# Performance work log

Measured on AMD Instinct MI355X. Metric: run time of the kernel, lower is better.

The kernel has to match this reference:

```python
import jax, jax.numpy as jnp
import numpy as np

D_MODEL = 1024
HEAD_DIM = 256
MEMORY_SIZE = 64
SPARSITY_RATIO = 0.1
NEG_INF = -1.0e9


def setup_inputs() -> dict:
    key = jax.random.key(0)
    ks = jax.random.split(key, 16)
    s = lambda fan_in: 1.0 / np.sqrt(fan_in)
    inp = {
        "x": jax.random.normal(ks[0], (2, 4096, D_MODEL), dtype=jnp.float32),
        # local attention head (qkv fused, no bias); weights stored [in, out]
        "local_qkv_w": jax.random.uniform(ks[1], (D_MODEL, 3 * HEAD_DIM), minval=-s(D_MODEL), maxval=s(D_MODEL)),
        # sparse global head
        "sparse_qkv_w": jax.random.uniform(ks[2], (D_MODEL, 3 * HEAD_DIM), minval=-s(D_MODEL), maxval=s(D_MODEL)),
        # memory head
        "memory_bank": jax.random.normal(ks[3], (MEMORY_SIZE, HEAD_DIM), dtype=jnp.float32),
        "memory_proj_w": jax.random.uniform(ks[4], (D_MODEL, HEAD_DIM), minval=-s(D_MODEL), maxval=s(D_MODEL)),
        "mem_out_w": jax.random.uniform(ks[5], (2 * HEAD_DIM, HEAD_DIM), minval=-s(2 * HEAD_DIM), maxval=s(2 * HEAD_DIM)),
        "mem_out_b": jax.random.uniform(ks[6], (HEAD_DIM,), minval=-s(2 * HEAD_DIM), maxval=s(2 * HEAD_DIM)),
        # prediction head
        "pred_in_w": jax.random.uniform(ks[7], (D_MODEL, HEAD_DIM), minval=-s(D_MODEL), maxval=s(D_MODEL)),
        "pred_in_b": jax.random.uniform(ks[8], (HEAD_DIM,), minval=-s(D_MODEL), maxval=s(D_MODEL)),
        "pred1_w": jax.random.uniform(ks[9], (HEAD_DIM, 2 * HEAD_DIM), minval=-s(HEAD_DIM), maxval=s(HEAD_DIM)),
        "pred1_b": jax.random.uniform(ks[10], (2 * HEAD_DIM,), minval=-s(HEAD_DIM), maxval=s(HEAD_DIM)),
        "pred2_w": jax.random.uniform(ks[11], (2 * HEAD_DIM, HEAD_DIM), minval=-s(2 * HEAD_DIM), maxval=s(2 * HEAD_DIM)),
        "pred2_b": jax.random.uniform(ks[12], (HEAD_DIM,), minval=-s(2 * HEAD_DIM), maxval=s(2 * HEAD_DIM)),
        # warboss output projection
        "warboss_w": jax.random.uniform(ks[13], (4 * HEAD_DIM, D_MODEL), minval=-s(4 * HEAD_DIM), maxval=s(4 * HEAD_DIM)),
        "warboss_b": jax.random.uniform(ks[14], (D_MODEL,), minval=-s(4 * HEAD_DIM), maxval=s(4 * HEAD_DIM)),
    }
    return inp


def _full_attention(x, qkv_w, scale):
    # x: [B,S,D] -> q,k,v: [B,S,H]
    qkv = x @ qkv_w
    q, k, v = jnp.split(qkv, 3, axis=-1)
    scores = jnp.einsum("bsh,bth->bst", q, k) * scale  # [B,S,S]
    probs = jax.nn.softmax(scores, axis=-1)
    return probs @ v


def _sparse_global_attention(x, qkv_w, scale):
    qkv = x @ qkv_w
    q, k, v = jnp.split(qkv, 3, axis=-1)
    scores = jnp.einsum("bsh,bth->bst", q, k) * scale  # [B,S,S]
    seq_len = x.shape[1]
    k_sparse = max(1, int(seq_len * SPARSITY_RATIO))
    topk_vals, _ = jax.lax.top_k(scores, k_sparse)
    kth = topk_vals[..., -1:]  # [B,S,1] threshold
    masked = jnp.where(scores >= kth, scores, NEG_INF)
    probs = jax.nn.softmax(masked, axis=-1)
    return probs @ v


def _memory_head(x, memory_bank, memory_proj_w, mem_out_w, mem_out_b):
    x_proj = x @ memory_proj_w  # [B,S,H]
    mem_scores = jnp.einsum("bsh,mh->bsm", x_proj, memory_bank)
    mem_weights = jax.nn.softmax(mem_scores, axis=-1)
    retrieved = jnp.einsum("bsm,mh->bsh", mem_weights, memory_bank)
    combined = jnp.concatenate([x_proj, retrieved], axis=-1)
    return combined @ mem_out_w + mem_out_b


def _prediction_head(x, pred_in_w, pred_in_b, pred1_w, pred1_b, pred2_w, pred2_b):
    h = x @ pred_in_w + pred_in_b
    h = h @ pred1_w + pred1_b
    h = jax.nn.gelu(h, approximate=False)
    return h @ pred2_w + pred2_b


def reference(x, local_qkv_w, sparse_qkv_w, memory_bank, memory_proj_w, mem_out_w, mem_out_b, pred_in_w, pred_in_b, pred1_w, pred1_b, pred2_w, pred2_b, warboss_w, warboss_b):
    scale = HEAD_DIM ** -0.5
    local_out = _full_attention(x, local_qkv_w, scale)
    sparse_out = _sparse_global_attention(x, sparse_qkv_w, scale)
    mem_out = _memory_head(x, memory_bank, memory_proj_w, mem_out_w, mem_out_b)
    pred_out = _prediction_head(x, pred_in_w, pred_in_b, pred1_w, pred1_b, pred2_w, pred2_b)
    combined = jnp.concatenate([local_out, sparse_out, mem_out, pred_out], axis=-1)
    return combined @ warboss_w + warboss_b
```

## Files before the change

kernel.cpp:

```cpp
#include <hip/hip_runtime.h>
#include <hip/hip_bf16.h>

typedef __attribute__((ext_vector_type(8))) _Float16 half8;
typedef __attribute__((ext_vector_type(4))) _Float16 half4v;
typedef __attribute__((ext_vector_type(4))) float f32x4;

__device__ __forceinline__ float wred_max(float v){
  #pragma unroll
  for (int o = 32; o; o >>= 1) v = fmaxf(v, __shfl_xor(v, o));
  return v;
}
__device__ __forceinline__ float wred_sum(float v){
  #pragma unroll
  for (int o = 32; o; o >>= 1) v += __shfl_xor(v, o);
  return v;
}
__device__ __forceinline__ unsigned short h2u(_Float16 h){
  unsigned short u;
  __builtin_memcpy(&u, &h, 2);
  return u;
}
__device__ __forceinline__ float u2hf(unsigned short u){
  _Float16 h;
  __builtin_memcpy(&h, &u, 2);
  return (float)h;
}

#define GLOAD16(GP, LP) __builtin_amdgcn_global_load_lds( \
    (const __attribute__((address_space(1))) void*)(GP),  \
    (__attribute__((address_space(3))) void*)(LP), 16, 0, 0)

template<int BM, int BN, int OUT_F16, int ACT>
__global__ __launch_bounds__(256) void gemm_ht(
    const _Float16* __restrict__ A, long saz, int lda,
    const _Float16* __restrict__ B, long sbz, int ldb,
    void* __restrict__ Cv, long scz, int ldc,
    int K, float alpha, const float* __restrict__ bias)
{
  constexpr int FM = BM / 32, FN = BN / 32;
  __shared__ __align__(16) _Float16 Asl[BM * 32];
  __shared__ __align__(16) _Float16 Bsl[BN * 32];
  const int t = threadIdx.x;
  const int wid = t >> 6, lane = t & 63;
  const int wr = wid >> 1, wc = wid & 1;
  const int lr = lane & 15, kg = lane >> 4;
  A += (long)blockIdx.z * saz;
  B += (long)blockIdx.z * sbz;
  const long row0 = (long)blockIdx.y * BM;
  const long col0 = (long)blockIdx.x * BN;

  f32x4 acc[FM][FN];
  #pragma unroll
  for (int i = 0; i < FM; i++)
    #pragma unroll
    for (int j = 0; j < FN; j++)
      acc[i][j] = (f32x4){0.f, 0.f, 0.f, 0.f};

  const int arow_t = t >> 2, acol_t = (t & 3) * 8;

  for (int k0 = 0; k0 < K; k0 += 32){
    #pragma unroll
    for (int r = 0; r < BM / 64; r++){
      const _Float16* gp = A + (row0 + r*64 + arow_t) * (long)lda + k0 + acol_t;
      GLOAD16(gp, (char*)Asl + r*4096 + wid*1024);
    }
    #pragma unroll
    for (int r = 0; r < BN / 64; r++){
      const _Float16* gp = B + (col0 + r*64 + arow_t) * (long)ldb + k0 + acol_t;
      GLOAD16(gp, (char*)Bsl + r*4096 + wid*1024);
    }
    __syncthreads();
    half8 af[FM], bfv[FN];
    #pragma unroll
    for (int i = 0; i < FM; i++)
      af[i] = *(const half8*)((const char*)Asl + (wr*(BM/2) + i*16 + lr)*64 + kg*16);
    #pragma unroll
    for (int j = 0; j < FN; j++)
      bfv[j] = *(const half8*)((const char*)Bsl + (wc*(BN/2) + j*16 + lr)*64 + kg*16);
    #pragma unroll
    for (int i = 0; i < FM; i++)
      #pragma unroll
      for (int j = 0; j < FN; j++)
        acc[i][j] = __builtin_amdgcn_mfma_f32_16x16x32_f16(af[i], bfv[j], acc[i][j], 0, 0, 0);
    __syncthreads();
  }

  _Float16* Ch = (_Float16*)Cv + (long)blockIdx.z * scz;
  float*    Cf = (float*)Cv    + (long)blockIdx.z * scz;
  #pragma unroll
  for (int i = 0; i < FM; i++){
    #pragma unroll
    for (int j = 0; j < FN; j++){
      #pragma unroll
      for (int q = 0; q < 4; q++){
        long rr = row0 + wr*(BM/2) + i*16 + kg*4 + q;
        long cc = col0 + wc*(BN/2) + j*16 + lr;
        float val = acc[i][j][q] * alpha;
        if (bias) val += bias[cc];
        if constexpr (ACT) val = 0.5f * val * (1.0f + erff(val * 0.70710678118654752f));
        if constexpr (OUT_F16) Ch[rr*(long)ldc + cc] = (_Float16)val;
        else                   Cf[rr*(long)ldc + cc] = val;
      }
    }
  }
}

template<int BM, int BN, int SPARSE>
__global__ __launch_bounds__(256) void gemm_pv_exp(
    const _Float16* __restrict__ A, long saz, int lda,
    const _Float16* __restrict__ B, long sbz, int ldb,
    const float4* __restrict__ mlthr,
    _Float16* __restrict__ Ph, int nsplit, int Ksplit)
{
  constexpr int FM = BM / 32, FN = BN / 32;
  __shared__ __align__(16) _Float16 Asl[BM * 32];
  __shared__ __align__(16) _Float16 Bsl[BN * 32];
  const int t = threadIdx.x;
  const int wid = t >> 6, lane = t & 63;
  const int wr = wid >> 1, wc = wid & 1;
  const int lr = lane & 15, kg = lane >> 4;
  const int z = blockIdx.z, batch = z / nsplit, split = z % nsplit;
  A += (long)batch * saz;
  B += (long)batch * sbz;
  _Float16* Pz = Ph + (size_t)z * (4096 * 256);
  const long row0 = (long)blockIdx.y * BM;
  const int Kbase = split * Ksplit;

  const long arow = row0 + (t >> 2);
  const float4 mt = mlthr[(long)batch*4096 + arow];
  const float m = mt.x, thr = mt.z;
  const _Float16* Ap = A + arow * (long)lda + Kbase + (t & 3) * 8;

  f32x4 acc[FM][FN];
  #pragma unroll
  for (int i = 0; i < FM; i++)
    #pragma unroll
    for (int j = 0; j < FN; j++)
      acc[i][j] = (f32x4){0.f, 0.f, 0.f, 0.f};

  const int arow_t = t >> 2, acol_t = (t & 3) * 8;

  for (int k0 = 0; k0 < Ksplit; k0 += 32){
    #pragma unroll
    for (int r = 0; r < BN / 64; r++){
      const _Float16* gp = B + (r*64 + arow_t) * (long)ldb + Kbase + k0 + acol_t;
      GLOAD16(gp, (char*)Bsl + r*4096 + wid*1024);
    }
    {
      half8 ld = *(const half8*)(Ap + k0);
      half8 st;
      #pragma unroll
      for (int e = 0; e < 8; e++){
        float v = (float)ld[e];
        float ev;
        if constexpr (SPARSE) ev = (v >= thr) ? __expf(v - m) : 0.f;
        else                  ev = __expf(v - m);
        st[e] = (_Float16)ev;
      }
      *(half8*)((char*)Asl + t*16) = st;
    }
    __syncthreads();
    half8 af[FM], bfv[FN];
    #pragma unroll
    for (int i = 0; i < FM; i++)
      af[i] = *(const half8*)((const char*)Asl + (wr*(BM/2) + i*16 + lr)*64 + kg*16);
    #pragma unroll
    for (int j = 0; j < FN; j++)
      bfv[j] = *(const half8*)((const char*)Bsl + (wc*(BN/2) + j*16 + lr)*64 + kg*16);
    #pragma unroll
    for (int i = 0; i < FM; i++)
      #pragma unroll
      for (int j = 0; j < FN; j++)
        acc[i][j] = __builtin_amdgcn_mfma_f32_16x16x32_f16(af[i], bfv[j], acc[i][j], 0, 0, 0);
    __syncthreads();
  }

  #pragma unroll
  for (int i = 0; i < FM; i++)
    #pragma unroll
    for (int j = 0; j < FN; j++)
      #pragma unroll
      for (int q = 0; q < 4; q++){
        long rr = row0 + wr*(BM/2) + i*16 + kg*4 + q;
        long cc = wc*(BN/2) + j*16 + lr;
        Pz[rr*256 + cc] = (_Float16)acc[i][j][q];
      }
}

__global__ __launch_bounds__(256) void reduce4h(const _Float16* __restrict__ Ph,
                                                const float4* __restrict__ mlthr,
                                                _Float16* __restrict__ dst, int coff, int nq){
  int i = blockIdx.x * 256 + threadIdx.x;
  if (i >= nq) return;
  int b = i >> 18;
  int r = i & 262143;
  int row = r >> 6, col4 = r & 63;
  float sx = 0.f, sy = 0.f, sz = 0.f, sw = 0.f;
  #pragma unroll
  for (int sp = 0; sp < 4; sp++){
    half4v p = *(const half4v*)(Ph + (((size_t)(b*4 + sp)*4096 + row)*256 + col4*4));
    sx += (float)p[0]; sy += (float)p[1]; sz += (float)p[2]; sw += (float)p[3];
  }
  const float inv = 1.0f / mlthr[(long)b*4096 + row].y;
  half4v o;
  o[0] = (_Float16)(sx*inv); o[1] = (_Float16)(sy*inv);
  o[2] = (_Float16)(sz*inv); o[3] = (_Float16)(sw*inv);
  *(half4v*)(dst + ((size_t)b*4096 + row)*1024 + coff + col4*4) = o;
}

__global__ __launch_bounds__(256) void cast_xh(const float* __restrict__ in,
                                               _Float16* __restrict__ out, int n8){
  int i = blockIdx.x * 256 + threadIdx.x;
  const int stride = gridDim.x * 256;
  for (; i < n8; i += stride){
    float4 a = ((const float4*)in)[2*i];
    float4 b = ((const float4*)in)[2*i + 1];
    half8 o;
    o[0]=(_Float16)a.x; o[1]=(_Float16)a.y; o[2]=(_Float16)a.z; o[3]=(_Float16)a.w;
    o[4]=(_Float16)b.x; o[5]=(_Float16)b.y; o[6]=(_Float16)b.z; o[7]=(_Float16)b.w;
    *(half8*)(out + (size_t)i*8) = o;
  }
}

__global__ __launch_bounds__(256) void transpose_cast_w(const float* __restrict__ in, int R, int C,
                                                        _Float16* __restrict__ out){
  __shared__ float tile[32][33];
  const int c0 = blockIdx.x * 32, r0 = blockIdx.y * 32;
  const int tx = threadIdx.x & 31, ty = threadIdx.x >> 5;
  #pragma unroll
  for (int i = 0; i < 32; i += 8)
    tile[ty+i][tx] = in[(size_t)(r0+ty+i)*C + c0+tx];
  __syncthreads();
  #pragma unroll
  for (int i = 0; i < 32; i += 8)
    out[(size_t)(c0+ty+i)*R + r0+tx] = (_Float16)tile[tx][ty+i];
}

__global__ __launch_bounds__(256) void transpose_h(
    const _Float16* __restrict__ in, long in_z, int ld_in,
    _Float16* __restrict__ out, long out_z, int ld_out)
{
  __shared__ _Float16 tile[32][34];
  const _Float16* ip = in + (long)blockIdx.z * in_z;
  _Float16* op = out + (long)blockIdx.z * out_z;
  const int c0 = blockIdx.x * 32, r0 = blockIdx.y * 32;
  const int tx = threadIdx.x & 31, ty = threadIdx.x >> 5;
  #pragma unroll
  for (int i = 0; i < 32; i += 8)
    tile[ty+i][tx] = ip[(long)(r0+ty+i)*ld_in + c0+tx];
  __syncthreads();
  #pragma unroll
  for (int i = 0; i < 32; i += 8)
    op[(long)(c0+ty+i)*ld_out + r0+tx] = tile[tx][ty+i];
}

__global__ __launch_bounds__(256) void rowstat_local(const _Float16* __restrict__ sc,
                                                     float4* __restrict__ mlthr){
  __shared__ float red[4], red2[4];
  const int t = threadIdx.x, lane = t & 63, wid = t >> 6;
  const _Float16* p = sc + (size_t)blockIdx.x * 4096;
  half8 a = ((const half8*)p)[t*2];
  half8 b = ((const half8*)p)[t*2 + 1];
  float v[16];
  #pragma unroll
  for (int e = 0; e < 8; e++){ v[e] = (float)a[e]; v[8+e] = (float)b[e]; }
  float m = v[0];
  #pragma unroll
  for (int e = 1; e < 16; e++) m = fmaxf(m, v[e]);
  m = wred_max(m);
  if (lane == 0) red[wid] = m;
  __syncthreads();
  m = fmaxf(fmaxf(red[0], red[1]), fmaxf(red[2], red[3]));
  float s = 0.f;
  #pragma unroll
  for (int e = 0; e < 16; e++) s += __expf(v[e] - m);
  s = wred_sum(s);
  if (lane == 0) red2[wid] = s;
  __syncthreads();
  if (t == 0){
    s = red2[0] + red2[1] + red2[2] + red2[3];
    mlthr[blockIdx.x] = make_float4(m, s, -3.0e38f, 0.f);
  }
}

__global__ __launch_bounds__(256) void rowstat_sparse(const _Float16* __restrict__ sc,
                                                      float4* __restrict__ mlthr, int ksel){
  __shared__ unsigned hist4[4][256];
  __shared__ unsigned hrev[256];
  __shared__ unsigned suf[257];
  __shared__ unsigned wtot[4];
  __shared__ int selb;
  __shared__ float red[4], red2[4];
  const int t = threadIdx.x, lane = t & 63, wid = t >> 6;
  const _Float16* p = sc + (size_t)blockIdx.x * 4096;
  half8 a = ((const half8*)p)[t*2];
  half8 b = ((const half8*)p)[t*2 + 1];
  float v[16]; unsigned kk[16];
  #pragma unroll
  for (int e = 0; e < 8; e++){
    unsigned short u0 = h2u(a[e]);
    unsigned short u1 = h2u(b[e]);
    kk[e]   = (u0 & 0x8000u) ? (unsigned)(unsigned short)~u0 : (unsigned)(u0 | 0x8000u);
    kk[8+e] = (u1 & 0x8000u) ? (unsigned)(unsigned short)~u1 : (unsigned)(u1 | 0x8000u);
    v[e] = (float)a[e]; v[8+e] = (float)b[e];
  }
  float m = v[0];
  #pragma unroll
  for (int e = 1; e < 16; e++) m = fmaxf(m, v[e]);
  m = wred_max(m);
  if (lane == 0) red[wid] = m;
  __syncthreads();
  m = fmaxf(fmaxf(red[0], red[1]), fmaxf(red[2], red[3]));

  ((uint4*)hist4)[t] = (uint4){0u,0u,0u,0u};
  __syncthreads();
  #pragma unroll
  for (int e = 0; e < 16; e++) atomicAdd(&hist4[wid][kk[e] >> 8], 1u);
  __syncthreads();
  hrev[t] = hist4[0][t] + hist4[1][t] + hist4[2][t] + hist4[3][t];
  __syncthreads();
  unsigned x = hrev[255 - t];
  #pragma unroll
  for (int o = 1; o < 64; o <<= 1){
    unsigned y = __shfl_up(x, o);
    if (lane >= o) x += y;
  }
  if (lane == 63) wtot[wid] = x;
  __syncthreads();
  #pragma unroll
  for (int w = 0; w < 4; w++) if (w < wid) x += wtot[w];
  suf[255 - t] = x;
  if (t == 0) suf[256] = 0u;
  __syncthreads();
  const unsigned ku = (unsigned)ksel;
  if (suf[t] >= ku && suf[t+1] < ku) selb = t;
  __syncthreads();
  const int b1 = selb;
  const unsigned rem = ku - suf[b1+1];
  __syncthreads();

  ((uint4*)hist4)[t] = (uint4){0u,0u,0u,0u};
  __syncthreads();
  #pragma unroll
  for (int e = 0; e < 16; e++)
    if ((int)(kk[e] >> 8) == b1) atomicAdd(&hist4[wid][kk[e] & 255u], 1u);
  __syncthreads();
  hrev[t] = hist4[0][t] + hist4[1][t] + hist4[2][t] + hist4[3][t];
  __syncthreads();
  x = hrev[255 - t];
  #pragma unroll
  for (int o = 1; o < 64; o <<= 1){
    unsigned y = __shfl_up(x, o);
    if (lane >= o) x += y;
  }
  if (lane == 63) wtot[wid] = x;
  __syncthreads();
  #pragma unroll
  for (int w = 0; w < 4; w++) if (w < wid) x += wtot[w];
  suf[255 - t] = x;
  if (t == 0) suf[256] = 0u;
  __syncthreads();
  if (suf[t] >= rem && suf[t+1] < rem) selb = t;
  __syncthreads();
  const unsigned Tkey = ((unsigned)b1 << 8) | (unsigned)selb;
  const unsigned short tu = (Tkey & 0x8000u) ? (unsigned short)(Tkey & 0x7fffu)
                                             : (unsigned short)~Tkey;
  const float thr = u2hf(tu);

  float s = 0.f;
  #pragma unroll
  for (int e = 0; e < 16; e++)
    s += (v[e] >= thr) ? __expf(v[e] - m) : 0.f;
  s = wred_sum(s);
  if (lane == 0) red2[wid] = s;
  __syncthreads();
  if (t == 0){
    s = red2[0] + red2[1] + red2[2] + red2[3];
    mlthr[blockIdx.x] = make_float4(m, s, thr, 0.f);
  }
}

__global__ __launch_bounds__(256) void msoftmax64(const float* __restrict__ mscore,
                                                  _Float16* __restrict__ mprob){
  const int t = threadIdx.x, lane = t & 63, wid = t >> 6;
  const size_t row = (size_t)blockIdx.x * 4 + wid;
  float v = mscore[row*64 + lane];
  float m = wred_max(v);
  float e = expf(v - m);
  float s = wred_sum(e);
  mprob[row*64 + lane] = (_Float16)(e / s);
}

extern "C" void kernel_launch(void* const* d_in, const int* in_sizes, int n_in,
                              void* d_out, int out_size, void* d_ws, size_t ws_size,
                              hipStream_t stream)
{
  const float* x             = (const float*)d_in[0];
  const float* local_qkv_w   = (const float*)d_in[1];
  const float* sparse_qkv_w  = (const float*)d_in[2];
  const float* memory_bank   = (const float*)d_in[3];
  const float* memory_proj_w = (const float*)d_in[4];
  const float* mem_out_w     = (const float*)d_in[5];
  const float* mem_out_b     = (const float*)d_in[6];
  const float* pred_in_w     = (const float*)d_in[7];
  const float* pred_in_b     = (const float*)d_in[8];
  const float* pred1_w       = (const float*)d_in[9];
  const float* pred1_b       = (const float*)d_in[10];
  const float* pred2_w       = (const float*)d_in[11];
  const float* pred2_b       = (const float*)d_in[12];
  const float* warboss_w     = (const float*)d_in[13];
  const float* warboss_b     = (const float*)d_in[14];
  float* out = (float*)d_out;
  _Float16* Ph = (_Float16*)d_out;

  char* wsb = (char*)d_ws;
  _Float16*  scores_h = (_Float16*)wsb;
  _Float16*  x_h      = (_Float16*)wsb;
  _Float16*  mem_cat  = (_Float16*)(wsb + 16777216);
  _Float16*  h_in     = (_Float16*)(wsb + 25165824);
  _Float16*  h1       = (_Float16*)(wsb + 29360128);
  float*     mscore   = (float*)(wsb + 37748736);
  _Float16*  mprob    = (_Float16*)(wsb + 39845888);
  _Float16*  qkv_l    = (_Float16*)(wsb + 67108864);
  _Float16*  qkv_s    = (_Float16*)(wsb + 79691776);
  _Float16*  Vt       = (_Float16*)(wsb + 92274688);
  _Float16*  comb     = (_Float16*)(wsb + 96468992);
  _Float16*  lqkvT    = (_Float16*)(wsb + 113246208);
  _Float16*  sqkvT    = lqkvT  + 786432;
  _Float16*  mprojT   = sqkvT  + 786432;
  _Float16*  moutT    = mprojT + 262144;
  _Float16*  pinT     = moutT  + 131072;
  _Float16*  p1T      = pinT   + 262144;
  _Float16*  p2T      = p1T    + 131072;
  _Float16*  wbT      = p2T    + 131072;
  _Float16*  bank_h   = wbT    + 1048576;
  _Float16*  bankT_h  = bank_h + 16384;
  float4*    mlthr    = (float4*)(bankT_h + 16384);

  const dim3 blk(256);
  const float scale = 0.0625f;
  const long QZ  = (long)4096 * 768;
  const long VZ  = (long)256 * 4096;
  const long SZH = (long)4096 * 4096;

  cast_xh<<<dim3(2048), blk, 0, stream>>>(x, x_h, 1048576);
  cast_xh<<<dim3(8), blk, 0, stream>>>(memory_bank, bank_h, 2048);
  transpose_cast_w<<<dim3(24,32), blk, 0, stream>>>(local_qkv_w,  1024,  768, lqkvT);
  transpose_cast_w<<<dim3(24,32), blk, 0, stream>>>(sparse_qkv_w, 1024,  768, sqkvT);
  transpose_cast_w<<<dim3( 8,32), blk, 0, stream>>>(memory_proj_w,1024,  256, mprojT);
  transpose_cast_w<<<dim3( 8,16), blk, 0, stream>>>(mem_out_w,     512,  256, moutT);
  transpose_cast_w<<<dim3( 8,32), blk, 0, stream>>>(pred_in_w,    1024,  256, pinT);
  transpose_cast_w<<<dim3(16, 8), blk, 0, stream>>>(pred1_w,       256,  512, p1T);
  transpose_cast_w<<<dim3( 8,16), blk, 0, stream>>>(pred2_w,       512,  256, p2T);
  transpose_cast_w<<<dim3(32,32), blk, 0, stream>>>(warboss_w,    1024, 1024, wbT);
  transpose_cast_w<<<dim3( 8, 2), blk, 0, stream>>>(memory_bank,    64,  256, bankT_h);

  gemm_ht<128,128,1,0><<<dim3(6,64,2), blk, 0, stream>>>(x_h,0,1024, lqkvT,786432,1024,
                                                         qkv_l,6291456,768, 1024, 1.f, nullptr);

  gemm_ht<64,64,1,0><<<dim3(4,128), blk, 0, stream>>>(x_h,0,1024, mprojT,0,1024, mem_cat,0,512, 1024, 1.f, nullptr);
  gemm_ht<64,64,0,0><<<dim3(1,128), blk, 0, stream>>>(mem_cat,0,512, bank_h,0,256, (void*)mscore,0,64, 256, 1.f, nullptr);
  msoftmax64<<<dim3(2048), blk, 0, stream>>>(mscore, mprob);
  gemm_ht<64,64,1,0><<<dim3(4,128), blk, 0, stream>>>(mprob,0,64, bankT_h,0,64, mem_cat+256,0,512, 64, 1.f, nullptr);
  gemm_ht<64,64,1,0><<<dim3(4,128), blk, 0, stream>>>(mem_cat,0,512, moutT,0,512, comb+512,0,1024, 512, 1.f, mem_out_b);

  gemm_ht<64,64,1,0><<<dim3(4,128), blk, 0, stream>>>(x_h,0,1024, pinT,0,1024, h_in,0,256, 1024, 1.f, pred_in_b);
  gemm_ht<64,128,1,1><<<dim3(4,128), blk, 0, stream>>>(h_in,0,256, p1T,0,256, h1,0,512, 256, 1.f, pred1_b);
  gemm_ht<64,64,1,0><<<dim3(4,128), blk, 0, stream>>>(h1,0,512, p2T,0,512, comb+768,0,1024, 512, 1.f, pred2_b);

  transpose_h<<<dim3(8,128,2), blk, 0, stream>>>(qkv_l+512, QZ, 768, Vt, VZ, 4096);
  gemm_ht<128,128,1,0><<<dim3(32,32,2), blk, 0, stream>>>(qkv_l,QZ,768, qkv_l+256,QZ,768,
                                                          (void*)scores_h,SZH,4096, 256, scale, nullptr);
  rowstat_local<<<dim3(8192), blk, 0, stream>>>(scores_h, mlthr);
  gemm_pv_exp<64,256,0><<<dim3(1,64,8), blk, 0, stream>>>(scores_h,SZH,4096, Vt,VZ,4096, mlthr, Ph, 4, 1024);
  reduce4h<<<dim3(2048), blk, 0, stream>>>(Ph, mlthr, comb, 0, 524288);

  transpose_h<<<dim3(8,128,2), blk, 0, stream>>>(qkv_s+512, QZ, 768, Vt, VZ, 4096);
  gemm_ht<128,128,1,0><<<dim3(32,32,2), blk, 0, stream>>>(qkv_s,QZ,768, qkv_s+256,QZ,768,
                                                          (void*)scores_h,SZH,4096, 256, scale, nullptr);
  rowstat_sparse<<<dim3(8192), blk, 0, stream>>>(scores_h, mlthr, 409);
  gemm_pv_exp<64,256,1><<<dim3(1,64,8), blk, 0, stream>>>(scores_h,SZH,4096, Vt,VZ,4096, mlthr, Ph, 4, 1024);
  reduce4h<<<dim3(2048), blk, 0, stream>>>(Ph, mlthr, comb, 256, 524288);

  gemm_ht<128,128,0,0><<<dim3(8,64), blk, 0, stream>>>(comb,0,1024, wbT,0,1024, (void*)out,0,1024, 1024, 1.f, warboss_b);
}
```

Before: 403.1 us.

## Double-buffer LDS tiles in GEMM kernels to overlap loads with MFMA

Both the generic fp16 GEMM and the fused exp-weighted PV GEMM now use two LDS buffers per operand. The next K-tile is issued via global_load_lds, or loaded and exponentiated into the alternate buffer, while MFMAs run on the current one. One barrier per iteration replaces two. This is meant to hide global memory latency behind compute, at the cost of doubled shared memory, which may reduce occupancy.

```diff
diff --git a/kernel.cpp b/kernel.cpp
--- a/kernel.cpp
+++ b/kernel.cpp
@@ -38,8 +38,8 @@
     int K, float alpha, const float* __restrict__ bias)
 {
   constexpr int FM = BM / 32, FN = BN / 32;
-  __shared__ __align__(16) _Float16 Asl[BM * 32];
-  __shared__ __align__(16) _Float16 Bsl[BN * 32];
+  __shared__ __align__(16) _Float16 Asl[2][BM * 32];
+  __shared__ __align__(16) _Float16 Bsl[2][BN * 32];
   const int t = threadIdx.x;
   const int wid = t >> 6, lane = t & 63;
   const int wr = wid >> 1, wc = wid & 1;
@@ -49,6 +49,21 @@
   const long row0 = (long)blockIdx.y * BM;
   const long col0 = (long)blockIdx.x * BN;
 
+  const int arow_t = t >> 2, acol_t = (t & 3) * 8;
+
+  auto stage = [&](int buf, int k0){
+    #pragma unroll
+    for (int r = 0; r < BM / 64; r++){
+      const _Float16* gp = A + (row0 + r*64 + arow_t) * (long)lda + k0 + acol_t;
+      GLOAD16(gp, (char*)Asl[buf] + r*4096 + wid*1024);
+    }
+    #pragma unroll
+    for (int r = 0; r < BN / 64; r++){
+      const _Float16* gp = B + (col0 + r*64 + arow_t) * (long)ldb + k0 + acol_t;
+      GLOAD16(gp, (char*)Bsl[buf] + r*4096 + wid*1024);
+    }
+  };
+
   f32x4 acc[FM][FN];
   #pragma unroll
   for (int i = 0; i < FM; i++)
@@ -56,33 +71,25 @@
     for (int j = 0; j < FN; j++)
       acc[i][j] = (f32x4){0.f, 0.f, 0.f, 0.f};
 
-  const int arow_t = t >> 2, acol_t = (t & 3) * 8;
-
+  stage(0, 0);
+  __syncthreads();
+  int cur = 0;
   for (int k0 = 0; k0 < K; k0 += 32){
-    #pragma unroll
-    for (int r = 0; r < BM / 64; r++){
-      const _Float16* gp = A + (row0 + r*64 + arow_t) * (long)lda + k0 + acol_t;
-      GLOAD16(gp, (char*)Asl + r*4096 + wid*1024);
-    }
-    #pragma unroll
-    for (int r = 0; r < BN / 64; r++){
-      const _Float16* gp = B + (col0 + r*64 + arow_t) * (long)ldb + k0 + acol_t;
-      GLOAD16(gp, (char*)Bsl + r*4096 + wid*1024);
-    }
-    __syncthreads();
+    if (k0 + 32 < K) stage(cur ^ 1, k0 + 32);
     half8 af[FM], bfv[FN];
     #pragma unroll
     for (int i = 0; i < FM; i++)
-      af[i] = *(const half8*)((const char*)Asl + (wr*(BM/2) + i*16 + lr)*64 + kg*16);
+      af[i] = *(const half8*)((const char*)Asl[cur] + (wr*(BM/2) + i*16 + lr)*64 + kg*16);
     #pragma unroll
     for (int j = 0; j < FN; j++)
-      bfv[j] = *(const half8*)((const char*)Bsl + (wc*(BN/2) + j*16 + lr)*64 + kg*16);
+      bfv[j] = *(const half8*)((const char*)Bsl[cur] + (wc*(BN/2) + j*16 + lr)*64 + kg*16);
     #pragma unroll
     for (int i = 0; i < FM; i++)
       #pragma unroll
       for (int j = 0; j < FN; j++)
         acc[i][j] = __builtin_amdgcn_mfma_f32_16x16x32_f16(af[i], bfv[j], acc[i][j], 0, 0, 0);
     __syncthreads();
+    cur ^= 1;
   }
 
   _Float16* Ch = (_Float16*)Cv + (long)blockIdx.z * scz;
@@ -113,8 +120,8 @@
     _Float16* __restrict__ Ph, int nsplit, int Ksplit)
 {
   constexpr int FM = BM / 32, FN = BN / 32;
-  __shared__ __align__(16) _Float16 Asl[BM * 32];
-  __shared__ __align__(16) _Float16 Bsl[BN * 32];
+  __shared__ __align__(16) _Float16 Asl[2][BM * 32];
+  __shared__ __align__(16) _Float16 Bsl[2][BN * 32];
   const int t = threadIdx.x;
   const int wid = t >> 6, lane = t & 63;
   const int wr = wid >> 1, wc = wid & 1;
@@ -131,6 +138,28 @@
   const float m = mt.x, thr = mt.z;
   const _Float16* Ap = A + arow * (long)lda + Kbase + (t & 3) * 8;
 
+  const int arow_t = t >> 2, acol_t = (t & 3) * 8;
+
+  auto stageB = [&](int buf, int k0){
+    #pragma unroll
+    for (int r = 0; r < BN / 64; r++){
+      const _Float16* gp = B + (r*64 + arow_t) * (long)ldb + Kbase + k0 + acol_t;
+      GLOAD16(gp, (char*)Bsl[buf] + r*4096 + wid*1024);
+    }
+  };
+  auto expw = [&](int buf, half8 ld){
+    half8 st;
+    #pragma unroll
+    for (int e = 0; e < 8; e++){
+      float v = (float)ld[e];
+      float ev;
+      if constexpr (SPARSE) ev = (v >= thr) ? __expf(v - m) : 0.f;
+      else                  ev = __expf(v - m);
+      st[e] = (_Float16)ev;
+    }
+    *(half8*)((char*)Asl[buf] + t*16) = st;
+  };
+
   f32x4 acc[FM][FN];
   #pragma unroll
   for (int i = 0; i < FM; i++)
@@ -138,41 +167,32 @@
     for (int j = 0; j < FN; j++)
       acc[i][j] = (f32x4){0.f, 0.f, 0.f, 0.f};
 
-  const int arow_t = t >> 2, acol_t = (t & 3) * 8;
-
+  stageB(0, 0);
+  expw(0, *(const half8*)(Ap + 0));
+  __syncthreads();
+  int cur = 0;
   for (int k0 = 0; k0 < Ksplit; k0 += 32){
-    #pragma unroll
-    for (int r = 0; r < BN / 64; r++){
-      const _Float16* gp = B + (r*64 + arow_t) * (long)ldb + Kbase + k0 + acol_t;
-      GLOAD16(gp, (char*)Bsl + r*4096 + wid*1024);
+    const bool more = (k0 + 32 < Ksplit);
+    half8 lda_next;
+    if (more){
+      stageB(cur ^ 1, k0 + 32);
+      lda_next = *(const half8*)(Ap + k0 + 32);
     }
-    {
-      half8 ld = *(const half8*)(Ap + k0);
-      half8 st;
-      #pragma unroll
-      for (int e = 0; e < 8; e++){
-        float v = (float)ld[e];
-        float ev;
-        if constexpr (SPARSE) ev = (v >= thr) ? __expf(v - m) : 0.f;
-        else                  ev = __expf(v - m);
-        st[e] = (_Float16)ev;
-      }
-      *(half8*)((char*)Asl + t*16) = st;
-    }
-    __syncthreads();
     half8 af[FM], bfv[FN];
     #pragma unroll
     for (int i = 0; i < FM; i++)
-      af[i] = *(const half8*)((const char*)Asl + (wr*(BM/2) + i*16 + lr)*64 + kg*16);
+      af[i] = *(const half8*)((const char*)Asl[cur] + (wr*(BM/2) + i*16 + lr)*64 + kg*16);
     #pragma unroll
     for (int j = 0; j < FN; j++)
-      bfv[j] = *(const half8*)((const char*)Bsl + (wc*(BN/2) + j*16 + lr)*64 + kg*16);
+      bfv[j] = *(const half8*)((const char*)Bsl[cur] + (wc*(BN/2) + j*16 + lr)*64 + kg*16);
     #pragma unroll
     for (int i = 0; i < FM; i++)
       #pragma unroll
       for (int j = 0; j < FN; j++)
         acc[i][j] = __builtin_amdgcn_mfma_f32_16x16x32_f16(af[i], bfv[j], acc[i][j], 0, 0, 0);
+    if (more) expw(cur ^ 1, lda_next);
     __syncthreads();
+    cur ^= 1;
   }
 
   #pragma unroll
```

Measured after the change: 390.6 us. 3.1% less time.
